# Kernel optimization log

Measured on AMD Instinct MI355X. Metric: run time of the kernel, lower is better.

The kernel has to match this reference:

```python
import jax, jax.numpy as jnp
import numpy as np

N, IN_F, OUT_F = 65536, 512, 512


def setup_inputs() -> dict:
    key = jax.random.key(0)
    k1, k2, k3 = jax.random.split(key, 3)
    # Activations arrive as dequant-pending uint8-valued floats in [0, 256).
    x = jax.random.randint(k1, (N, IN_F), 0, 256).astype(jnp.float32)
    weight = jax.random.randint(k2, (OUT_F, IN_F), 0, 256).astype(jnp.int32)
    bias = jax.random.randint(k3, (OUT_F,), -512, 512).astype(jnp.int32)
    return {
        "x": x,
        "weight": weight,
        "bias": bias,
        "M": jnp.asarray(0.0123, dtype=jnp.float32),
        "x_zero": jnp.asarray(128.0, dtype=jnp.float32),
        "w_zero": jnp.asarray(128.0, dtype=jnp.float32),
        "y_zero": jnp.asarray(128.0, dtype=jnp.float32),
    }


def reference(x, weight, bias, M, x_zero, w_zero, y_zero):
    # y = round(linear(x - x_zero, w - w_zero, b) * M + y_zero)
    xs = x - x_zero                                   # [N, IN_F]
    w = weight.astype(jnp.float32) - w_zero           # [OUT_F, IN_F]
    y = jnp.einsum("ni,oi->no", xs, w) + bias.astype(jnp.float32)
    return jnp.round(y * M + y_zero)
```

## Files before the change

### kernel.cpp

```cpp
#include <hip/hip_runtime.h>


#define K_DIM 512
#define OUTF  512
#define NT    8
#define B_OFF 4096
#define BUF_B (4096 + 32768)

typedef __attribute__((ext_vector_type(4))) int   i32x4;
typedef __attribute__((ext_vector_type(4))) float f32x4;
typedef __attribute__((ext_vector_type(2))) unsigned int u32x2;

__device__ __forceinline__ void gload16(const void* g, void* l) {
    __builtin_amdgcn_global_load_lds(
        (const __attribute__((address_space(1))) void*)g,
        (__attribute__((address_space(3))) void*)l, 16, 0, 0);
}

__global__ void wprep(const int* __restrict__ W, unsigned int* __restrict__ Wb,
                      const float* __restrict__ wzp) {
    const int wz = __float2int_rn(wzp[0]);
    int idx = (blockIdx.x * blockDim.x + threadIdx.x) * 4;
    i32x4 w = *reinterpret_cast<const i32x4*>(W + idx);
    unsigned int p = ((unsigned int)(w[0] - wz) & 0xffu)
                   | (((unsigned int)(w[1] - wz) & 0xffu) << 8)
                   | (((unsigned int)(w[2] - wz) & 0xffu) << 16)
                   | (((unsigned int)(w[3] - wz) & 0xffu) << 24);
    Wb[idx >> 2] = p;
}

__global__ __launch_bounds__(512, 4)
void qgemm(const float* __restrict__ X,
           const unsigned char* __restrict__ Wb,
           const int* __restrict__ bias,
           const float* __restrict__ Mp,
           const float* __restrict__ xzp,
           const float* __restrict__ yzp,
           float* __restrict__ Y) {
    __shared__ unsigned char lds[2][BUF_B];

    const int tid  = threadIdx.x;
    const int lane = tid & 63;
    const int wid  = tid >> 6;
    const int wr   = wid >> 2;
    const int wc   = wid & 3;
    const int fr   = lane & 15;
    const int fq   = lane >> 4;

    const int row0 = blockIdx.x * 64;

    const float xzf = xzp[0];

    const int arow  = tid >> 3;
    const int kslot = tid & 7;
    const float* xbase = X + (size_t)(row0 + arow) * K_DIM + kslot * 8;
    const int dA = (arow >> 4) * 1024 + (((arow & 15) + ((kslot >> 1) << 4)) << 4)
                 + ((kslot & 1) << 3);

    const unsigned char* wbase = Wb + (size_t)(wid * 64 + fr) * K_DIM + fq * 16;
    const int ldsB = B_OFF + wid * 4096;

    f32x4 ra[2][2];

    auto stageA = [&](int t) {
        const int s = t & 1;
        const float* p = xbase + t * 64;
        ra[s][0] = *reinterpret_cast<const f32x4*>(p);
        ra[s][1] = *reinterpret_cast<const f32x4*>(p + 4);
    };
    auto gloadB = [&](int t, int buf) {
        const unsigned char* g = wbase + t * 64;
        #pragma unroll
        for (int f = 0; f < 4; ++f)
            gload16(g + (size_t)f * 16 * K_DIM, &lds[buf][ldsB + f * 1024]);
    };
    auto convwriteA = [&](int t) {
        const int s = t & 1;
        u32x2 v;
        #pragma unroll
        for (int h = 0; h < 2; ++h) {
            unsigned int u0 = (unsigned int)((int)(ra[s][h][0] - xzf)) & 0xffu;
            unsigned int u1 = (unsigned int)((int)(ra[s][h][1] - xzf)) & 0xffu;
            unsigned int u2 = (unsigned int)((int)(ra[s][h][2] - xzf)) & 0xffu;
            unsigned int u3 = (unsigned int)((int)(ra[s][h][3] - xzf)) & 0xffu;
            v[h] = u0 | (u1 << 8) | (u2 << 16) | (u3 << 24);
        }
        *reinterpret_cast<u32x2*>(&lds[s][dA]) = v;
    };

    const int c0 = wc * 128;
    i32x4 acc[2][8];
    #pragma unroll
    for (int n = 0; n < 8; ++n) {
        const int bv = bias[c0 + n * 16 + fr];
        acc[0][n] = i32x4{bv, bv, bv, bv};
        acc[1][n] = i32x4{bv, bv, bv, bv};
    }

    const int aBase = (wr * 2) * 1024 + lane * 16;
    const int bBase = B_OFF + (wc * 8) * 1024 + lane * 16;

    auto compute = [&](int t) {
        const int s = t & 1;
        i32x4 af0 = *reinterpret_cast<const i32x4*>(&lds[s][aBase]);
        i32x4 af1 = *reinterpret_cast<const i32x4*>(&lds[s][aBase + 1024]);
        #pragma unroll
        for (int n = 0; n < 8; ++n) {
            i32x4 bf = *reinterpret_cast<const i32x4*>(&lds[s][bBase + n * 1024]);
            acc[0][n] = __builtin_amdgcn_mfma_i32_16x16x64_i8(af0, bf, acc[0][n], 0, 0, 0);
            acc[1][n] = __builtin_amdgcn_mfma_i32_16x16x64_i8(af1, bf, acc[1][n], 0, 0, 0);
        }
    };

    stageA(0);
    stageA(1);
    gloadB(0, 0);
    convwriteA(0);
    __syncthreads();

    #pragma unroll
    for (int t = 0; t < NT; ++t) {
        if (t + 2 < NT) stageA(t + 2);
        if (t + 1 < NT) gloadB(t + 1, (t + 1) & 1);
        compute(t);
        if (t + 1 < NT) convwriteA(t + 1);
        __syncthreads();
    }

    const float Mv = Mp[0], yz = yzp[0];
    #pragma unroll
    for (int m = 0; m < 2; ++m) {
        const int row = row0 + wr * 32 + m * 16 + fq * 4;
        #pragma unroll
        for (int n = 0; n < 8; ++n) {
            float* yp = Y + (size_t)row * OUTF + c0 + n * 16 + fr;
            #pragma unroll
            for (int j = 0; j < 4; ++j)
                yp[(size_t)j * OUTF] = rintf((float)acc[m][n][j] * Mv + yz);
        }
    }
}

extern "C" void kernel_launch(void* const* d_in, const int* in_sizes, int n_in,
                              void* d_out, int out_size, void* d_ws, size_t ws_size,
                              hipStream_t stream) {
    const float* x    = (const float*)d_in[0];
    const int*   w    = (const int*)d_in[1];
    const int*   bias = (const int*)d_in[2];
    const float* M    = (const float*)d_in[3];
    const float* xz   = (const float*)d_in[4];
    const float* wz   = (const float*)d_in[5];
    const float* yz   = (const float*)d_in[6];
    float* y = (float*)d_out;

    unsigned int* Wb = (unsigned int*)d_ws;

    wprep<<<256, 256, 0, stream>>>(w, Wb, wz);
    qgemm<<<1024, 512, 0, stream>>>(x, (const unsigned char*)Wb, bias, M, xz, yz, y);
}
```

Baseline: 74.67 us.

## Preload full A tile, halve block rows, per-wave B double-buffering without barriers

Each block now handles 32 rows. It converts the whole 32x512 activation slice to int8 in LDS once, up front, instead of streaming it through a software pipeline. Each wave then owns a 64-column slice of weights and double-buffers its own B tiles with direct global-to-LDS loads, synchronising through explicit vmcnt waits instead of block-wide barriers in the K loop. The aim is to remove per-step __syncthreads and the A conversion from the inner loop, and to double the grid for more parallelism. The cost is twice the weight traffic per output row, a larger LDS footprint (about 80KB per block) that limits resident blocks, and reliance on in-wave ordering for reusing the B buffers.

```diff
diff --git a/kernel.cpp b/kernel.cpp
--- a/kernel.cpp
+++ b/kernel.cpp
@@ -4,12 +4,10 @@
 #define K_DIM 512
 #define OUTF  512
 #define NT    8
-#define B_OFF 4096
-#define BUF_B (4096 + 32768)
+#define B_OFF 16384
 
 typedef __attribute__((ext_vector_type(4))) int   i32x4;
 typedef __attribute__((ext_vector_type(4))) float f32x4;
-typedef __attribute__((ext_vector_type(2))) unsigned int u32x2;
 
 __device__ __forceinline__ void gload16(const void* g, void* l) {
     __builtin_amdgcn_global_load_lds(
@@ -29,6 +27,23 @@
     Wb[idx >> 2] = p;
 }
 
+__device__ __forceinline__ int pack16(const f32x4 v0, const f32x4 v1,
+                                      const f32x4 v2, const f32x4 v3,
+                                      float xzf, i32x4* out) {
+    const f32x4 vv[4] = {v0, v1, v2, v3};
+    i32x4 p;
+    #pragma unroll
+    for (int q = 0; q < 4; ++q) {
+        unsigned int u0 = (unsigned int)((int)(vv[q][0] - xzf)) & 0xffu;
+        unsigned int u1 = (unsigned int)((int)(vv[q][1] - xzf)) & 0xffu;
+        unsigned int u2 = (unsigned int)((int)(vv[q][2] - xzf)) & 0xffu;
+        unsigned int u3 = (unsigned int)((int)(vv[q][3] - xzf)) & 0xffu;
+        p[q] = (int)(u0 | (u1 << 8) | (u2 << 16) | (u3 << 24));
+    }
+    *out = p;
+    return 0;
+}
+
 __global__ __launch_bounds__(512, 4)
 void qgemm(const float* __restrict__ X,
            const unsigned char* __restrict__ Wb,
@@ -37,103 +52,88 @@
            const float* __restrict__ xzp,
            const float* __restrict__ yzp,
            float* __restrict__ Y) {
-    __shared__ unsigned char lds[2][BUF_B];
+    __shared__ unsigned char lds[B_OFF + 8 * 8192];
 
     const int tid  = threadIdx.x;
     const int lane = tid & 63;
     const int wid  = tid >> 6;
-    const int wr   = wid >> 2;
-    const int wc   = wid & 3;
     const int fr   = lane & 15;
     const int fq   = lane >> 4;
 
-    const int row0 = blockIdx.x * 64;
+    const int row0 = blockIdx.x * 32;
 
     const float xzf = xzp[0];
 
-    const int arow  = tid >> 3;
-    const int kslot = tid & 7;
-    const float* xbase = X + (size_t)(row0 + arow) * K_DIM + kslot * 8;
-    const int dA = (arow >> 4) * 1024 + (((arow & 15) + ((kslot >> 1) << 4)) << 4)
-                 + ((kslot & 1) << 3);
+    {
+        const int s0 = tid * 2;
+        const int gA = s0 >> 9;
+        const int tA = (s0 >> 6) & 7;
+        const int l0 = s0 & 63;
+        const int r0 = 16 * gA + (l0 & 15);
+        const int k0 = 64 * tA + ((l0 >> 4) << 4);
+        const float* xa = X + (size_t)(row0 + r0) * K_DIM + k0;
+        f32x4 va[4], vb[4];
+        #pragma unroll
+        for (int q = 0; q < 4; ++q) va[q] = *reinterpret_cast<const f32x4*>(xa + q * 4);
+        #pragma unroll
+        for (int q = 0; q < 4; ++q) vb[q] = *reinterpret_cast<const f32x4*>(xa + K_DIM + q * 4);
+        i32x4 pa, pb;
+        pack16(va[0], va[1], va[2], va[3], xzf, &pa);
+        pack16(vb[0], vb[1], vb[2], vb[3], xzf, &pb);
+        *reinterpret_cast<i32x4*>(&lds[s0 * 16])      = pa;
+        *reinterpret_cast<i32x4*>(&lds[s0 * 16 + 16]) = pb;
+    }
 
-    const unsigned char* wbase = Wb + (size_t)(wid * 64 + fr) * K_DIM + fq * 16;
-    const int ldsB = B_OFF + wid * 4096;
-
-    f32x4 ra[2][2];
-
-    auto stageA = [&](int t) {
-        const int s = t & 1;
-        const float* p = xbase + t * 64;
-        ra[s][0] = *reinterpret_cast<const f32x4*>(p);
-        ra[s][1] = *reinterpret_cast<const f32x4*>(p + 4);
-    };
-    auto gloadB = [&](int t, int buf) {
-        const unsigned char* g = wbase + t * 64;
-        #pragma unroll
-        for (int f = 0; f < 4; ++f)
-            gload16(g + (size_t)f * 16 * K_DIM, &lds[buf][ldsB + f * 1024]);
-    };
-    auto convwriteA = [&](int t) {
-        const int s = t & 1;
-        u32x2 v;
-        #pragma unroll
-        for (int h = 0; h < 2; ++h) {
-            unsigned int u0 = (unsigned int)((int)(ra[s][h][0] - xzf)) & 0xffu;
-            unsigned int u1 = (unsigned int)((int)(ra[s][h][1] - xzf)) & 0xffu;
-            unsigned int u2 = (unsigned int)((int)(ra[s][h][2] - xzf)) & 0xffu;
-            unsigned int u3 = (unsigned int)((int)(ra[s][h][3] - xzf)) & 0xffu;
-            v[h] = u0 | (u1 << 8) | (u2 << 16) | (u3 << 24);
-        }
-        *reinterpret_cast<u32x2*>(&lds[s][dA]) = v;
-    };
-
-    const int c0 = wc * 128;
-    i32x4 acc[2][8];
+    i32x4 acc[2][4];
     #pragma unroll
-    for (int n = 0; n < 8; ++n) {
-        const int bv = bias[c0 + n * 16 + fr];
+    for (int n = 0; n < 4; ++n) {
+        const int bv = bias[wid * 64 + n * 16 + fr];
         acc[0][n] = i32x4{bv, bv, bv, bv};
         acc[1][n] = i32x4{bv, bv, bv, bv};
     }
 
-    const int aBase = (wr * 2) * 1024 + lane * 16;
-    const int bBase = B_OFF + (wc * 8) * 1024 + lane * 16;
+    __syncthreads();
 
-    auto compute = [&](int t) {
-        const int s = t & 1;
-        i32x4 af0 = *reinterpret_cast<const i32x4*>(&lds[s][aBase]);
-        i32x4 af1 = *reinterpret_cast<const i32x4*>(&lds[s][aBase + 1024]);
+    const unsigned char* wbase = Wb + (size_t)(wid * 64 + fr) * K_DIM + fq * 16;
+    const int bBuf = B_OFF + wid * 8192;
+
+    auto gloadB = [&](int t) {
+        const unsigned char* g = wbase + t * 64;
+        const int d = bBuf + (t & 1) * 4096;
+        gload16(g,                &lds[d]);
+        gload16(g + 16 * K_DIM,   &lds[d + 1024]);
+        gload16(g + 32 * K_DIM,   &lds[d + 2048]);
+        gload16(g + 48 * K_DIM,   &lds[d + 3072]);
+    };
+
+    gloadB(0);
+
+    #pragma unroll
+    for (int t = 0; t < NT; ++t) {
+        if (t + 1 < NT) {
+            gloadB(t + 1);
+            asm volatile("s_waitcnt vmcnt(4)" ::: "memory");
+        } else {
+            asm volatile("s_waitcnt vmcnt(0)" ::: "memory");
+        }
+        i32x4 af0 = *reinterpret_cast<const i32x4*>(&lds[((0 * 8 + t) * 64 + lane) * 16]);
+        i32x4 af1 = *reinterpret_cast<const i32x4*>(&lds[((1 * 8 + t) * 64 + lane) * 16]);
+        const int bb = bBuf + (t & 1) * 4096 + lane * 16;
         #pragma unroll
-        for (int n = 0; n < 8; ++n) {
-            i32x4 bf = *reinterpret_cast<const i32x4*>(&lds[s][bBase + n * 1024]);
+        for (int n = 0; n < 4; ++n) {
+            i32x4 bf = *reinterpret_cast<const i32x4*>(&lds[bb + n * 1024]);
             acc[0][n] = __builtin_amdgcn_mfma_i32_16x16x64_i8(af0, bf, acc[0][n], 0, 0, 0);
             acc[1][n] = __builtin_amdgcn_mfma_i32_16x16x64_i8(af1, bf, acc[1][n], 0, 0, 0);
         }
-    };
-
-    stageA(0);
-    stageA(1);
-    gloadB(0, 0);
-    convwriteA(0);
-    __syncthreads();
-
-    #pragma unroll
-    for (int t = 0; t < NT; ++t) {
-        if (t + 2 < NT) stageA(t + 2);
-        if (t + 1 < NT) gloadB(t + 1, (t + 1) & 1);
-        compute(t);
-        if (t + 1 < NT) convwriteA(t + 1);
-        __syncthreads();
     }
 
     const float Mv = Mp[0], yz = yzp[0];
     #pragma unroll
     for (int m = 0; m < 2; ++m) {
-        const int row = row0 + wr * 32 + m * 16 + fq * 4;
+        const int row = row0 + m * 16 + fq * 4;
         #pragma unroll
-        for (int n = 0; n < 8; ++n) {
-            float* yp = Y + (size_t)row * OUTF + c0 + n * 16 + fr;
+        for (int n = 0; n < 4; ++n) {
+            float* yp = Y + (size_t)row * OUTF + wid * 64 + n * 16 + fr;
             #pragma unroll
             for (int j = 0; j < 4; ++j)
                 yp[(size_t)j * OUTF] = rintf((float)acc[m][n][j] * Mv + yz);
@@ -156,5 +156,5 @@
     unsigned int* Wb = (unsigned int*)d_ws;
 
     wprep<<<256, 256, 0, stream>>>(w, Wb, wz);
-    qgemm<<<1024, 512, 0, stream>>>(x, (const unsigned char*)Wb, bias, M, xz, yz, y);
+    qgemm<<<2048, 512, 0, stream>>>(x, (const unsigned char*)Wb, bias, M, xz, yz, y);
 }
```

After: 100.8 us. +34.9%, slower.
